# Kernel optimization log

Hardware: AMD Instinct MI355X
Metric: run time of the kernel (lower is better)

Reference implementation:

```python
import jax, jax.numpy as jnp
import numpy as np

B, D, H, C = 128, 512, 1024, 1000


def setup_inputs() -> dict:
    key = jax.random.key(0)
    k1, k2, k3 = jax.random.split(key, 3)
    x = jax.random.normal(k1, (B, D), dtype=jnp.float32)
    W1 = jax.random.normal(k2, (D, H), dtype=jnp.float32) * (1.0 / np.sqrt(D))
    b1 = jnp.zeros((H,), dtype=jnp.float32)
    W2 = jax.random.normal(k3, (H, C), dtype=jnp.float32) * (1.0 / np.sqrt(H))
    b2 = jnp.zeros((C,), dtype=jnp.float32)
    return {"x": x, "W1": W1, "b1": b1, "W2": W2, "b2": b2, "step": 0}


def _logits(W1, b1, W2, b2, xi):
    # 2-layer MLP forward for a single sample xi: [D] -> [C]
    h = jnp.maximum(xi @ W1 + b1, 0.0)
    return h @ W2 + b2


def _per_sample_loss(params, xi, key):
    W1, b1, W2, b2 = params
    logit = _logits(W1, b1, W2, b2, xi)  # [C]
    # model samples a label from its own softmax (multinomial); sampling is
    # non-differentiable, matching torch's multinomial -> stop_gradient
    y = jax.random.categorical(key, jax.lax.stop_gradient(logit))
    return -jax.nn.log_softmax(logit)[y]  # CrossEntropyLoss on 1 sample


def reference(x, W1, b1, W2, b2, step):
    params = (W1, b1, W2, b2)
    keys = jax.random.split(jax.random.key(42), x.shape[0])
    # vmap(grad(loss)) -> per-sample gradients for every parameter
    grads = jax.vmap(jax.grad(_per_sample_loss), in_axes=(None, 0, 0))(params, x, keys)
    n = jnp.asarray(x.shape[0], dtype=x.dtype)
    # trace_p = sum_b ||g_b||^2 / B for each parameter
    traces = [jnp.sum(g * g) / n for g in grads]
    overall = traces[0] + traces[1] + traces[2] + traces[3]
    return jnp.stack([overall] + traces)  # [5]: overall, W1, b1, W2, b2
```

## Files before the change

kernel.cpp:

```cpp
#include <hip/hip_runtime.h>
#include <hip/hip_bf16.h>
#include <stdint.h>
#include <math.h>

#define B_N 128
#define D_N 512
#define H_N 1024
#define C_N 1000
#define CP  1024
#define NPART 8

__device__ __forceinline__ uint32_t rotl32(uint32_t v, int r) {
  return (v << r) | (v >> (32 - r));
}

__device__ __forceinline__ void threefry2x32(uint32_t k0, uint32_t k1,
                                             uint32_t x0, uint32_t x1,
                                             uint32_t &o0, uint32_t &o1) {
  uint32_t ks2 = k0 ^ k1 ^ 0x1BD11BDAu;
#define TF_R(r) { x0 += x1; x1 = rotl32(x1, r); x1 ^= x0; }
  x0 += k0; x1 += k1;
  TF_R(13) TF_R(15) TF_R(26) TF_R(6)
  x0 += k1; x1 += ks2 + 1u;
  TF_R(17) TF_R(29) TF_R(16) TF_R(24)
  x0 += ks2; x1 += k0 + 2u;
  TF_R(13) TF_R(15) TF_R(26) TF_R(6)
  x0 += k0; x1 += k1 + 3u;
  TF_R(17) TF_R(29) TF_R(16) TF_R(24)
  x0 += k1; x1 += ks2 + 4u;
  TF_R(13) TF_R(15) TF_R(26) TF_R(6)
  x0 += ks2; x1 += k0 + 5u;
#undef TF_R
  o0 = x0; o1 = x1;
}

__device__ __forceinline__ float gumbel_from_key(uint32_t k0, uint32_t k1, uint32_t i) {
  uint32_t o0, o1;
  threefry2x32(k0, k1, 0u, i, o0, o1);
  uint32_t bits = o0 ^ o1;
  uint32_t fb = (bits >> 9) | 0x3f800000u;
  float f = __uint_as_float(fb) - 1.0f;
  const float tiny = 1.1754943508222875e-38f;
  float u = fmaxf(tiny, f * (1.0f - tiny) + tiny);
  return -logf(-logf(u));
}

__device__ __forceinline__ float block_sum512(float v, float* red) {
  #pragma unroll
  for (int o = 32; o; o >>= 1) v += __shfl_xor(v, o);
  __syncthreads();
  if ((threadIdx.x & 63) == 0) red[threadIdx.x >> 6] = v;
  __syncthreads();
  return red[0] + red[1] + red[2] + red[3] + red[4] + red[5] + red[6] + red[7];
}

__device__ __forceinline__ float block_max512(float v, float* red) {
  #pragma unroll
  for (int o = 32; o; o >>= 1) v = fmaxf(v, __shfl_xor(v, o));
  __syncthreads();
  if ((threadIdx.x & 63) == 0) red[threadIdx.x >> 6] = v;
  __syncthreads();
  float m = red[0];
  #pragma unroll
  for (int w = 1; w < 8; w++) m = fmaxf(m, red[w]);
  return m;
}

__global__ __launch_bounds__(512) void k_fc1(const float* __restrict__ X,
                                             const float* __restrict__ W1,
                                             const float* __restrict__ b1,
                                             float* __restrict__ hpre) {
  __shared__ float xs[4 * D_N];
  int cbase = blockIdx.x * 128;
  int sbase = blockIdx.y * 4;
  int t = threadIdx.x;
  #pragma unroll
  for (int k = 0; k < 4; k++) {
    int idx = t + k * 512;
    xs[idx] = X[(sbase + (idx >> 9)) * D_N + (idx & 511)];
  }
  __syncthreads();
  int c = cbase + (t & 127);
  const float* xp = &xs[(t >> 7) * D_N];
  const float* W1c = W1 + c;
  float wA[16], wB[16];
  #pragma unroll
  for (int i = 0; i < 16; i++) wA[i] = W1c[i * H_N];
  float acc = 0.f;
  for (int d0 = 0; d0 < D_N; d0 += 32) {
    #pragma unroll
    for (int i = 0; i < 16; i++) wB[i] = W1c[((d0 + 16 + i) & (D_N - 1)) * H_N];
    #pragma unroll
    for (int q = 0; q < 4; q++) {
      float4 xa = *reinterpret_cast<const float4*>(&xp[d0 + q * 4]);
      acc += xa.x * wA[q*4+0] + xa.y * wA[q*4+1] + xa.z * wA[q*4+2] + xa.w * wA[q*4+3];
    }
    #pragma unroll
    for (int i = 0; i < 16; i++) wA[i] = W1c[((d0 + 32 + i) & (D_N - 1)) * H_N];
    #pragma unroll
    for (int q = 0; q < 4; q++) {
      float4 xa = *reinterpret_cast<const float4*>(&xp[d0 + 16 + q * 4]);
      acc += xa.x * wB[q*4+0] + xa.y * wB[q*4+1] + xa.z * wB[q*4+2] + xa.w * wB[q*4+3];
    }
  }
  hpre[(sbase + (t >> 7)) * H_N + c] = acc + b1[c];
}

__global__ __launch_bounds__(256) void k_fc2(const float* __restrict__ hpre,
                                             const float* __restrict__ W2,
                                             float* __restrict__ logits_part) {
  __shared__ float hs[8 * 128];
  int cbase = blockIdx.x * 128;
  int sbase = blockIdx.y * 8;
  int kb = blockIdx.z;
  int t = threadIdx.x;
  #pragma unroll
  for (int k = 0; k < 4; k++) {
    int idx = t + k * 256;
    hs[idx] = fmaxf(hpre[(sbase + (idx >> 7)) * H_N + kb * 128 + (idx & 127)], 0.0f);
  }
  __syncthreads();
  int c = cbase + (t & 127);
  if (c >= C_N) return;
  int sq = t >> 7;
  const float* hp0 = &hs[(sq * 4 + 0) * 128];
  const float* hp1 = &hs[(sq * 4 + 1) * 128];
  const float* hp2 = &hs[(sq * 4 + 2) * 128];
  const float* hp3 = &hs[(sq * 4 + 3) * 128];
  const float* W2c = W2 + (size_t)(kb * 128) * C_N + c;
  float wA[16], wB[16];
  #pragma unroll
  for (int i = 0; i < 16; i++) wA[i] = W2c[i * C_N];
  float a0 = 0.f, a1 = 0.f, a2 = 0.f, a3 = 0.f;
  for (int j0 = 0; j0 < 128; j0 += 32) {
    #pragma unroll
    for (int i = 0; i < 16; i++) wB[i] = W2c[((j0 + 16 + i) & 127) * C_N];
    #pragma unroll
    for (int q = 0; q < 4; q++) {
      float4 hA = *reinterpret_cast<const float4*>(&hp0[j0 + q * 4]);
      float4 hB = *reinterpret_cast<const float4*>(&hp1[j0 + q * 4]);
      float4 hC = *reinterpret_cast<const float4*>(&hp2[j0 + q * 4]);
      float4 hD = *reinterpret_cast<const float4*>(&hp3[j0 + q * 4]);
      a0 += hA.x * wA[q*4+0] + hA.y * wA[q*4+1] + hA.z * wA[q*4+2] + hA.w * wA[q*4+3];
      a1 += hB.x * wA[q*4+0] + hB.y * wA[q*4+1] + hB.z * wA[q*4+2] + hB.w * wA[q*4+3];
      a2 += hC.x * wA[q*4+0] + hC.y * wA[q*4+1] + hC.z * wA[q*4+2] + hC.w * wA[q*4+3];
      a3 += hD.x * wA[q*4+0] + hD.y * wA[q*4+1] + hD.z * wA[q*4+2] + hD.w * wA[q*4+3];
    }
    #pragma unroll
    for (int i = 0; i < 16; i++) wA[i] = W2c[((j0 + 32 + i) & 127) * C_N];
    #pragma unroll
    for (int q = 0; q < 4; q++) {
      float4 hA = *reinterpret_cast<const float4*>(&hp0[j0 + 16 + q * 4]);
      float4 hB = *reinterpret_cast<const float4*>(&hp1[j0 + 16 + q * 4]);
      float4 hC = *reinterpret_cast<const float4*>(&hp2[j0 + 16 + q * 4]);
      float4 hD = *reinterpret_cast<const float4*>(&hp3[j0 + 16 + q * 4]);
      a0 += hA.x * wB[q*4+0] + hA.y * wB[q*4+1] + hA.z * wB[q*4+2] + hA.w * wB[q*4+3];
      a1 += hB.x * wB[q*4+0] + hB.y * wB[q*4+1] + hB.z * wB[q*4+2] + hB.w * wB[q*4+3];
      a2 += hC.x * wB[q*4+0] + hC.y * wB[q*4+1] + hC.z * wB[q*4+2] + hC.w * wB[q*4+3];
      a3 += hD.x * wB[q*4+0] + hD.y * wB[q*4+1] + hD.z * wB[q*4+2] + hD.w * wB[q*4+3];
    }
  }
  float* lp = logits_part + (size_t)kb * (B_N * CP);
  int s0 = sbase + sq * 4;
  lp[(s0 + 0) * CP + c] = a0;
  lp[(s0 + 1) * CP + c] = a1;
  lp[(s0 + 2) * CP + c] = a2;
  lp[(s0 + 3) * CP + c] = a3;
}

__global__ __launch_bounds__(512) void k_sample(const float* __restrict__ X,
                                                const float* __restrict__ hpre,
                                                const float* __restrict__ logits_part,
                                                const float* __restrict__ b2,
                                                float* __restrict__ g,
                                                float* __restrict__ xsq_out,
                                                float* __restrict__ samp_part) {
  __shared__ float lg[C_N];
  __shared__ float red[8];
  __shared__ float redv[8];
  __shared__ int   redi[8];
  __shared__ uint32_t keys[2];
  int b = blockIdx.x;
  int t = threadIdx.x;

  {
    float sA = b2[t];
    float sB = (t + 512 < C_N) ? b2[t + 512] : 0.f;
    #pragma unroll
    for (int p = 0; p < NPART; p++) {
      const float* lp = logits_part + (size_t)p * (B_N * CP) + b * CP;
      sA += lp[t];
      if (t + 512 < C_N) sB += lp[t + 512];
    }
    lg[t] = sA;
    if (t + 512 < C_N) lg[t + 512] = sB;
  }
  if (t == 0) {
    uint32_t o0, o1;
    threefry2x32(0u, 42u, 0u, (uint32_t)b, o0, o1);
    keys[0] = o0; keys[1] = o1;
  }
  __syncthreads();
  uint32_t k0 = keys[0], k1 = keys[1];

  float bz = -INFINITY; int bi = 0x7fffffff;
  {
    float z0 = lg[t] + gumbel_from_key(k0, k1, (uint32_t)t);
    bz = z0; bi = t;
    if (t + 512 < C_N) {
      float z1 = lg[t + 512] + gumbel_from_key(k0, k1, (uint32_t)(t + 512));
      if (z1 > bz || (z1 == bz && (t + 512) < bi)) { bz = z1; bi = t + 512; }
    }
  }
  #pragma unroll
  for (int o = 32; o; o >>= 1) {
    float ov = __shfl_xor(bz, o);
    int   oi = __shfl_xor(bi, o);
    if (ov > bz || (ov == bz && oi < bi)) { bz = ov; bi = oi; }
  }
  if ((t & 63) == 0) { redv[t >> 6] = bz; redi[t >> 6] = bi; }
  __syncthreads();
  if (t == 0) {
    #pragma unroll
    for (int w = 1; w < 8; w++) {
      if (redv[w] > redv[0] || (redv[w] == redv[0] && redi[w] < redi[0])) {
        redv[0] = redv[w]; redi[0] = redi[w];
      }
    }
  }
  __syncthreads();
  int y = redi[0];

  float lm = lg[t];
  if (t + 512 < C_N) lm = fmaxf(lm, lg[t + 512]);
  float m = block_max512(lm, red);
  float ea = expf(lg[t] - m);
  float eb = (t + 512 < C_N) ? expf(lg[t + 512] - m) : 0.0f;
  float sum1 = block_sum512(ea + eb, red);
  float inv = 1.0f / sum1;

  float ga  = ea * inv - ((t == y) ? 1.0f : 0.0f);
  float gb2 = eb * inv - (((t + 512) == y) ? 1.0f : 0.0f);
  g[b * CP + t] = ga;
  g[b * CP + t + 512] = (t + 512 < C_N) ? gb2 : 0.0f;
  float gn = ga * ga + ((t + 512 < C_N) ? gb2 * gb2 : 0.0f);
  float tnorm = block_sum512(gn, red);

  float h0 = fmaxf(hpre[b * H_N + t], 0.0f);
  float h1 = fmaxf(hpre[b * H_N + t + 512], 0.0f);
  float hsq = block_sum512(h0 * h0 + h1 * h1, red);

  float xv = (t < D_N) ? X[b * D_N + t] : 0.0f;
  float xsq = block_sum512(xv * xv, red);

  if (t == 0) {
    xsq_out[b] = xsq;
    samp_part[b * 2 + 0] = hsq * tnorm;
    samp_part[b * 2 + 1] = tnorm;
  }
}

__global__ __launch_bounds__(512) void k_bwd1(const float* __restrict__ g,
                                              const float* __restrict__ W2,
                                              const float* __restrict__ hpre,
                                              const float* __restrict__ xsq,
                                              float* __restrict__ bwd_part) {
  __shared__ float gs[8 * 1024];
  __shared__ float xq[8];
  __shared__ float wred[8][2];
  int jb = blockIdx.x * 16;
  int sbase = blockIdx.y * 8;
  int t = threadIdx.x;
  #pragma unroll
  for (int k = 0; k < 16; k++) {
    int idx = t + k * 512;
    gs[idx] = g[(sbase + (idx >> 10)) * CP + (idx & 1023)];
  }
  if (t < 8) xq[t] = xsq[sbase + t];
  __syncthreads();

  int w = t >> 6, lane = t & 63;
  int j0 = jb + w * 2, j1 = j0 + 1;
  float a0[8] = {0,0,0,0,0,0,0,0};
  float a1[8] = {0,0,0,0,0,0,0,0};
  const float* w2r0 = W2 + (size_t)j0 * C_N;
  const float* w2r1 = W2 + (size_t)j1 * C_N;
  #pragma unroll
  for (int it = 0; it < 4; it++) {
    int c0 = it * 256 + lane * 4;
    bool act = (c0 < C_N);
    float4 wv0 = act ? *reinterpret_cast<const float4*>(w2r0 + c0)
                     : make_float4(0.f, 0.f, 0.f, 0.f);
    float4 wv1 = act ? *reinterpret_cast<const float4*>(w2r1 + c0)
                     : make_float4(0.f, 0.f, 0.f, 0.f);
    #pragma unroll
    for (int s = 0; s < 8; s++) {
      float4 gv = *reinterpret_cast<const float4*>(&gs[s * 1024 + c0]);
      a0[s] += wv0.x * gv.x + wv0.y * gv.y + wv0.z * gv.z + wv0.w * gv.w;
      a1[s] += wv1.x * gv.x + wv1.y * gv.y + wv1.z * gv.z + wv1.w * gv.w;
    }
  }
  #pragma unroll
  for (int off = 32; off; off >>= 1) {
    #pragma unroll
    for (int s = 0; s < 8; s++) {
      a0[s] += __shfl_xor(a0[s], off);
      a1[s] += __shfl_xor(a1[s], off);
    }
  }
  float cb = 0.f, cw = 0.f;
  #pragma unroll
  for (int s = 0; s < 8; s++) {
    float h0 = hpre[(sbase + s) * H_N + j0];
    float h1 = hpre[(sbase + s) * H_N + j1];
    float v0 = (h0 > 0.f) ? a0[s] : 0.f;
    float v1 = (h1 > 0.f) ? a1[s] : 0.f;
    float q = v0 * v0 + v1 * v1;
    cb += q;
    cw += xq[s] * q;
  }
  if (lane == 0) { wred[w][0] = cw; wred[w][1] = cb; }
  __syncthreads();
  if (t == 0) {
    float sw = 0.f, sb = 0.f;
    #pragma unroll
    for (int i = 0; i < 8; i++) { sw += wred[i][0]; sb += wred[i][1]; }
    int bid = blockIdx.y * 64 + blockIdx.x;
    bwd_part[bid * 2 + 0] = sw;
    bwd_part[bid * 2 + 1] = sb;
  }
}

__global__ __launch_bounds__(512) void k_final(const float* __restrict__ samp_part,
                                               const float* __restrict__ bwd_part,
                                               float* __restrict__ out) {
  __shared__ float red[8];
  int t = threadIdx.x;
  float w1v = bwd_part[t * 2 + 0] + bwd_part[(t + 512) * 2 + 0];
  float b1v = bwd_part[t * 2 + 1] + bwd_part[(t + 512) * 2 + 1];
  float w2v = (t < B_N) ? samp_part[t * 2 + 0] : 0.f;
  float b2v = (t < B_N) ? samp_part[t * 2 + 1] : 0.f;
  w1v = block_sum512(w1v, red);
  b1v = block_sum512(b1v, red);
  w2v = block_sum512(w2v, red);
  b2v = block_sum512(b2v, red);
  if (t == 0) {
    w1v /= 128.0f; b1v /= 128.0f; w2v /= 128.0f; b2v /= 128.0f;
    out[0] = w1v + b1v + w2v + b2v;
    out[1] = w1v;
    out[2] = b1v;
    out[3] = w2v;
    out[4] = b2v;
  }
}

extern "C" void kernel_launch(void* const* d_in, const int* in_sizes, int n_in,
                              void* d_out, int out_size, void* d_ws, size_t ws_size,
                              hipStream_t stream) {
  const float* X  = (const float*)d_in[0];
  const float* W1 = (const float*)d_in[1];
  const float* b1 = (const float*)d_in[2];
  const float* W2 = (const float*)d_in[3];
  const float* b2 = (const float*)d_in[4];
  float* out = (float*)d_out;

  float* ws        = (float*)d_ws;
  float* hpre      = ws;
  float* lpart     = hpre + 131072;
  float* g         = lpart + NPART * 131072;
  float* xsq       = g + 131072;
  float* samp_part = xsq + 128;
  float* bwd_part  = samp_part + 256;

  k_fc1<<<dim3(8, 32), 512, 0, stream>>>(X, W1, b1, hpre);
  k_fc2<<<dim3(8, 16, NPART), 256, 0, stream>>>(hpre, W2, lpart);
  k_sample<<<B_N, 512, 0, stream>>>(X, hpre, lpart, b2, g, xsq, samp_part);
  k_bwd1<<<dim3(64, 16), 512, 0, stream>>>(g, W2, hpre, xsq, bwd_part);
  k_final<<<1, 512, 0, stream>>>(samp_part, bwd_part, out);
}
```

Baseline: 57.43 us.

## Split-K register-tiled fc1/fc2 with 4x4 outer-product tiles and fused partial reduction

Rewrites the two forward GEMM kernels to compute 4 samples x 4 columns per thread from float4 weight loads and a transposed shared-memory activation tile. Both GEMMs are split along K into 16 partitions. The fc1 partials are summed, with bias and ReLU applied, when fc2 stages its input, and again in k_sample, which writes the final hidden pre-activations for the backward kernel. The aim is more register reuse and more blocks in flight for parallelism, at the cost of extra workspace traffic: 16 partial buffers for each layer that get reduced redundantly.

```diff
diff --git a/kernel.cpp b/kernel.cpp
--- a/kernel.cpp
+++ b/kernel.cpp
@@ -8,7 +8,8 @@
 #define H_N 1024
 #define C_N 1000
 #define CP  1024
-#define NPART 8
+#define NPART 16
+#define BH (B_N * H_N)
 
 __device__ __forceinline__ uint32_t rotl32(uint32_t v, int r) {
   return (v << r) | (v >> (32 - r));
@@ -66,113 +67,121 @@
   return m;
 }
 
-__global__ __launch_bounds__(512) void k_fc1(const float* __restrict__ X,
+__device__ __forceinline__ void fma4(float4 &a, const float4 &b, float s) {
+  a.x += b.x * s; a.y += b.y * s; a.z += b.z * s; a.w += b.w * s;
+}
+
+__global__ __launch_bounds__(256) void k_fc1(const float* __restrict__ X,
                                              const float* __restrict__ W1,
+                                             float* __restrict__ hpart) {
+  __shared__ float xT[32 * 20];
+  int cbase = blockIdx.x * 256;
+  int sbase = blockIdx.y * 16;
+  int dz = blockIdx.z;
+  int t = threadIdx.x;
+  {
+    int s = t >> 4;
+    int d2 = (t & 15) * 2;
+    float2 xv = *reinterpret_cast<const float2*>(
+        &X[(sbase + s) * D_N + dz * 32 + d2]);
+    xT[(d2 + 0) * 20 + s] = xv.x;
+    xT[(d2 + 1) * 20 + s] = xv.y;
+  }
+  __syncthreads();
+  int c4 = cbase + (t & 63) * 4;
+  int s4 = (t >> 6) * 4;
+  float4 acc0 = {0,0,0,0}, acc1 = {0,0,0,0}, acc2 = {0,0,0,0}, acc3 = {0,0,0,0};
+  const float* W1p = W1 + (size_t)(dz * 32) * H_N + c4;
+  float4 wb[4], wn[4];
+  #pragma unroll
+  for (int i = 0; i < 4; i++)
+    wb[i] = *reinterpret_cast<const float4*>(W1p + i * H_N);
+  for (int j0 = 0; j0 < 32; j0 += 4) {
+    #pragma unroll
+    for (int i = 0; i < 4; i++) {
+      int jn = j0 + 4 + i; jn = (jn < 32) ? jn : 31;
+      wn[i] = *reinterpret_cast<const float4*>(W1p + jn * H_N);
+    }
+    #pragma unroll
+    for (int i = 0; i < 4; i++) {
+      float4 xv = *reinterpret_cast<const float4*>(&xT[(j0 + i) * 20 + s4]);
+      fma4(acc0, wb[i], xv.x);
+      fma4(acc1, wb[i], xv.y);
+      fma4(acc2, wb[i], xv.z);
+      fma4(acc3, wb[i], xv.w);
+    }
+    #pragma unroll
+    for (int i = 0; i < 4; i++) wb[i] = wn[i];
+  }
+  float* hp = hpart + (size_t)dz * BH;
+  *reinterpret_cast<float4*>(&hp[(sbase + s4 + 0) * H_N + c4]) = acc0;
+  *reinterpret_cast<float4*>(&hp[(sbase + s4 + 1) * H_N + c4]) = acc1;
+  *reinterpret_cast<float4*>(&hp[(sbase + s4 + 2) * H_N + c4]) = acc2;
+  *reinterpret_cast<float4*>(&hp[(sbase + s4 + 3) * H_N + c4]) = acc3;
+}
+
+__global__ __launch_bounds__(256) void k_fc2(const float* __restrict__ hpart,
                                              const float* __restrict__ b1,
-                                             float* __restrict__ hpre) {
-  __shared__ float xs[4 * D_N];
-  int cbase = blockIdx.x * 128;
-  int sbase = blockIdx.y * 4;
-  int t = threadIdx.x;
-  #pragma unroll
-  for (int k = 0; k < 4; k++) {
-    int idx = t + k * 512;
-    xs[idx] = X[(sbase + (idx >> 9)) * D_N + (idx & 511)];
-  }
-  __syncthreads();
-  int c = cbase + (t & 127);
-  const float* xp = &xs[(t >> 7) * D_N];
-  const float* W1c = W1 + c;
-  float wA[16], wB[16];
-  #pragma unroll
-  for (int i = 0; i < 16; i++) wA[i] = W1c[i * H_N];
-  float acc = 0.f;
-  for (int d0 = 0; d0 < D_N; d0 += 32) {
-    #pragma unroll
-    for (int i = 0; i < 16; i++) wB[i] = W1c[((d0 + 16 + i) & (D_N - 1)) * H_N];
-    #pragma unroll
-    for (int q = 0; q < 4; q++) {
-      float4 xa = *reinterpret_cast<const float4*>(&xp[d0 + q * 4]);
-      acc += xa.x * wA[q*4+0] + xa.y * wA[q*4+1] + xa.z * wA[q*4+2] + xa.w * wA[q*4+3];
-    }
-    #pragma unroll
-    for (int i = 0; i < 16; i++) wA[i] = W1c[((d0 + 32 + i) & (D_N - 1)) * H_N];
-    #pragma unroll
-    for (int q = 0; q < 4; q++) {
-      float4 xa = *reinterpret_cast<const float4*>(&xp[d0 + 16 + q * 4]);
-      acc += xa.x * wB[q*4+0] + xa.y * wB[q*4+1] + xa.z * wB[q*4+2] + xa.w * wB[q*4+3];
-    }
-  }
-  hpre[(sbase + (t >> 7)) * H_N + c] = acc + b1[c];
-}
-
-__global__ __launch_bounds__(256) void k_fc2(const float* __restrict__ hpre,
                                              const float* __restrict__ W2,
-                                             float* __restrict__ logits_part) {
-  __shared__ float hs[8 * 128];
-  int cbase = blockIdx.x * 128;
-  int sbase = blockIdx.y * 8;
+                                             float* __restrict__ lpart) {
+  __shared__ float hT[64 * 20];
+  int cbase = blockIdx.x * 256;
+  int sbase = blockIdx.y * 16;
   int kb = blockIdx.z;
+  int jbase = kb * 64;
   int t = threadIdx.x;
   #pragma unroll
   for (int k = 0; k < 4; k++) {
     int idx = t + k * 256;
-    hs[idx] = fmaxf(hpre[(sbase + (idx >> 7)) * H_N + kb * 128 + (idx & 127)], 0.0f);
-  }
-  __syncthreads();
-  int c = cbase + (t & 127);
-  if (c >= C_N) return;
-  int sq = t >> 7;
-  const float* hp0 = &hs[(sq * 4 + 0) * 128];
-  const float* hp1 = &hs[(sq * 4 + 1) * 128];
-  const float* hp2 = &hs[(sq * 4 + 2) * 128];
-  const float* hp3 = &hs[(sq * 4 + 3) * 128];
-  const float* W2c = W2 + (size_t)(kb * 128) * C_N + c;
-  float wA[16], wB[16];
-  #pragma unroll
-  for (int i = 0; i < 16; i++) wA[i] = W2c[i * C_N];
-  float a0 = 0.f, a1 = 0.f, a2 = 0.f, a3 = 0.f;
-  for (int j0 = 0; j0 < 128; j0 += 32) {
-    #pragma unroll
-    for (int i = 0; i < 16; i++) wB[i] = W2c[((j0 + 16 + i) & 127) * C_N];
-    #pragma unroll
-    for (int q = 0; q < 4; q++) {
-      float4 hA = *reinterpret_cast<const float4*>(&hp0[j0 + q * 4]);
-      float4 hB = *reinterpret_cast<const float4*>(&hp1[j0 + q * 4]);
-      float4 hC = *reinterpret_cast<const float4*>(&hp2[j0 + q * 4]);
-      float4 hD = *reinterpret_cast<const float4*>(&hp3[j0 + q * 4]);
-      a0 += hA.x * wA[q*4+0] + hA.y * wA[q*4+1] + hA.z * wA[q*4+2] + hA.w * wA[q*4+3];
-      a1 += hB.x * wA[q*4+0] + hB.y * wA[q*4+1] + hB.z * wA[q*4+2] + hB.w * wA[q*4+3];
-      a2 += hC.x * wA[q*4+0] + hC.y * wA[q*4+1] + hC.z * wA[q*4+2] + hC.w * wA[q*4+3];
-      a3 += hD.x * wA[q*4+0] + hD.y * wA[q*4+1] + hD.z * wA[q*4+2] + hD.w * wA[q*4+3];
-    }
-    #pragma unroll
-    for (int i = 0; i < 16; i++) wA[i] = W2c[((j0 + 32 + i) & 127) * C_N];
-    #pragma unroll
-    for (int q = 0; q < 4; q++) {
-      float4 hA = *reinterpret_cast<const float4*>(&hp0[j0 + 16 + q * 4]);
-      float4 hB = *reinterpret_cast<const float4*>(&hp1[j0 + 16 + q * 4]);
-      float4 hC = *reinterpret_cast<const float4*>(&hp2[j0 + 16 + q * 4]);
-      float4 hD = *reinterpret_cast<const float4*>(&hp3[j0 + 16 + q * 4]);
-      a0 += hA.x * wB[q*4+0] + hA.y * wB[q*4+1] + hA.z * wB[q*4+2] + hA.w * wB[q*4+3];
-      a1 += hB.x * wB[q*4+0] + hB.y * wB[q*4+1] + hB.z * wB[q*4+2] + hB.w * wB[q*4+3];
-      a2 += hC.x * wB[q*4+0] + hC.y * wB[q*4+1] + hC.z * wB[q*4+2] + hC.w * wB[q*4+3];
-      a3 += hD.x * wB[q*4+0] + hD.y * wB[q*4+1] + hD.z * wB[q*4+2] + hD.w * wB[q*4+3];
-    }
-  }
-  float* lp = logits_part + (size_t)kb * (B_N * CP);
-  int s0 = sbase + sq * 4;
-  lp[(s0 + 0) * CP + c] = a0;
-  lp[(s0 + 1) * CP + c] = a1;
-  lp[(s0 + 2) * CP + c] = a2;
-  lp[(s0 + 3) * CP + c] = a3;
+    int s = idx >> 6, j = idx & 63;
+    float v = b1[jbase + j];
+    #pragma unroll
+    for (int p = 0; p < NPART; p++)
+      v += hpart[(size_t)p * BH + (sbase + s) * H_N + jbase + j];
+    hT[j * 20 + s] = fmaxf(v, 0.0f);
+  }
+  __syncthreads();
+  int c4 = cbase + (t & 63) * 4;
+  int s4 = (t >> 6) * 4;
+  if (c4 < C_N) {
+    float4 acc0 = {0,0,0,0}, acc1 = {0,0,0,0}, acc2 = {0,0,0,0}, acc3 = {0,0,0,0};
+    const float* W2p = W2 + (size_t)jbase * C_N + c4;
+    float4 wb[4], wn[4];
+    #pragma unroll
+    for (int i = 0; i < 4; i++)
+      wb[i] = *reinterpret_cast<const float4*>(W2p + (size_t)i * C_N);
+    for (int j0 = 0; j0 < 64; j0 += 4) {
+      #pragma unroll
+      for (int i = 0; i < 4; i++) {
+        int jn = j0 + 4 + i; jn = (jn < 64) ? jn : 63;
+        wn[i] = *reinterpret_cast<const float4*>(W2p + (size_t)jn * C_N);
+      }
+      #pragma unroll
+      for (int i = 0; i < 4; i++) {
+        float4 xv = *reinterpret_cast<const float4*>(&hT[(j0 + i) * 20 + s4]);
+        fma4(acc0, wb[i], xv.x);
+        fma4(acc1, wb[i], xv.y);
+        fma4(acc2, wb[i], xv.z);
+        fma4(acc3, wb[i], xv.w);
+      }
+      #pragma unroll
+      for (int i = 0; i < 4; i++) wb[i] = wn[i];
+    }
+    float* lp = lpart + (size_t)kb * (B_N * CP);
+    *reinterpret_cast<float4*>(&lp[(sbase + s4 + 0) * CP + c4]) = acc0;
+    *reinterpret_cast<float4*>(&lp[(sbase + s4 + 1) * CP + c4]) = acc1;
+    *reinterpret_cast<float4*>(&lp[(sbase + s4 + 2) * CP + c4]) = acc2;
+    *reinterpret_cast<float4*>(&lp[(sbase + s4 + 3) * CP + c4]) = acc3;
+  }
 }
 
 __global__ __launch_bounds__(512) void k_sample(const float* __restrict__ X,
-                                                const float* __restrict__ hpre,
-                                                const float* __restrict__ logits_part,
+                                                const float* __restrict__ hpart,
+                                                const float* __restrict__ b1,
+                                                const float* __restrict__ lpart,
                                                 const float* __restrict__ b2,
                                                 float* __restrict__ g,
+                                                float* __restrict__ hfinal,
                                                 float* __restrict__ xsq_out,
                                                 float* __restrict__ samp_part) {
   __shared__ float lg[C_N];
@@ -188,7 +197,7 @@
     float sB = (t + 512 < C_N) ? b2[t + 512] : 0.f;
     #pragma unroll
     for (int p = 0; p < NPART; p++) {
-      const float* lp = logits_part + (size_t)p * (B_N * CP) + b * CP;
+      const float* lp = lpart + (size_t)p * (B_N * CP) + b * CP;
       sA += lp[t];
       if (t + 512 < C_N) sB += lp[t + 512];
     }
@@ -246,9 +255,18 @@
   float gn = ga * ga + ((t + 512 < C_N) ? gb2 * gb2 : 0.0f);
   float tnorm = block_sum512(gn, red);
 
-  float h0 = fmaxf(hpre[b * H_N + t], 0.0f);
-  float h1 = fmaxf(hpre[b * H_N + t + 512], 0.0f);
-  float hsq = block_sum512(h0 * h0 + h1 * h1, red);
+  float h0 = b1[t];
+  float h1 = b1[t + 512];
+  #pragma unroll
+  for (int p = 0; p < NPART; p++) {
+    const float* hp = hpart + (size_t)p * BH + b * H_N;
+    h0 += hp[t];
+    h1 += hp[t + 512];
+  }
+  hfinal[b * H_N + t] = h0;
+  hfinal[b * H_N + t + 512] = h1;
+  float r0 = fmaxf(h0, 0.f), r1 = fmaxf(h1, 0.f);
+  float hsq = block_sum512(r0 * r0 + r1 * r1, red);
 
   float xv = (t < D_N) ? X[b * D_N + t] : 0.0f;
   float xsq = block_sum512(xv * xv, red);
@@ -262,7 +280,7 @@
 
 __global__ __launch_bounds__(512) void k_bwd1(const float* __restrict__ g,
                                               const float* __restrict__ W2,
-                                              const float* __restrict__ hpre,
+                                              const float* __restrict__ hfinal,
                                               const float* __restrict__ xsq,
                                               float* __restrict__ bwd_part) {
   __shared__ float gs[8 * 1024];
@@ -311,8 +329,8 @@
   float cb = 0.f, cw = 0.f;
   #pragma unroll
   for (int s = 0; s < 8; s++) {
-    float h0 = hpre[(sbase + s) * H_N + j0];
-    float h1 = hpre[(sbase + s) * H_N + j1];
+    float h0 = hfinal[(sbase + s) * H_N + j0];
+    float h1 = hfinal[(sbase + s) * H_N + j1];
     float v0 = (h0 > 0.f) ? a0[s] : 0.f;
     float v1 = (h1 > 0.f) ? a1[s] : 0.f;
     float q = v0 * v0 + v1 * v1;
@@ -365,16 +383,17 @@
   float* out = (float*)d_out;
 
   float* ws        = (float*)d_ws;
-  float* hpre      = ws;
-  float* lpart     = hpre + 131072;
-  float* g         = lpart + NPART * 131072;
-  float* xsq       = g + 131072;
+  float* hpart     = ws;
+  float* lpart     = hpart + NPART * BH;
+  float* g         = lpart + NPART * (B_N*CP);
+  float* hfinal    = g + (B_N * CP);
+  float* xsq       = hfinal + BH;
   float* samp_part = xsq + 128;
   float* bwd_part  = samp_part + 256;
 
-  k_fc1<<<dim3(8, 32), 512, 0, stream>>>(X, W1, b1, hpre);
-  k_fc2<<<dim3(8, 16, NPART), 256, 0, stream>>>(hpre, W2, lpart);
-  k_sample<<<B_N, 512, 0, stream>>>(X, hpre, lpart, b2, g, xsq, samp_part);
-  k_bwd1<<<dim3(64, 16), 512, 0, stream>>>(g, W2, hpre, xsq, bwd_part);
+  k_fc1<<<dim3(4, 8, NPART), 256, 0, stream>>>(X, W1, hpart);
+  k_fc2<<<dim3(4, 8, NPART), 256, 0, stream>>>(hpart, b1, W2, lpart);
+  k_sample<<<B_N, 512, 0, stream>>>(X, hpart, b1, lpart, b2, g, hfinal, xsq, samp_part);
+  k_bwd1<<<dim3(64, 16), 512, 0, stream>>>(g, W2, hfinal, xsq, bwd_part);
   k_final<<<1, 512, 0, stream>>>(samp_part, bwd_part, out);
 }
```

Result: no change. 57.68 us (+0.4%).
